# Performance work log

Hardware: AMD Instinct MI355X
Metric: run time of the kernel (lower is better)

Reference implementation:

```python
import jax, jax.numpy as jnp
import numpy as np

EPS = 1e-5

def bn_relu(y, g, b):
    # BatchNorm1d in training mode: stats over (B, L) per channel, biased variance
    mu = jnp.mean(y, axis=(0, 2), keepdims=True)
    var = jnp.var(y, axis=(0, 2), keepdims=True)
    yn = (y - mu) * jax.lax.rsqrt(var + EPS)
    return jax.nn.relu(yn * g[None, :, None] + b[None, :, None])

def conv1x1_pad1(x, W):
    # Conv1d(k=1, padding=1, bias=False): pointwise matmul then zero-pad length by 1 each side
    y = jnp.einsum('bcl,oc->bol', x, W)
    return jnp.pad(y, ((0, 0), (0, 0), (1, 1)))

def conv1x1(x, W, b):
    return jnp.einsum('bcl,oc->bol', x, W) + b[None, :, None]

def conv3_pad1(x, W):
    # Conv1d(k=3, padding=1, bias=False); W: [O, C, 3]
    return jax.lax.conv_general_dilated(x, W, window_strides=(1,), padding=((1, 1),),
                                        dimension_numbers=('NCH', 'OIH', 'NCH'))

def pam(f, Wq, bq, Wk, bk, Wv, bv, gamma):
    q = conv1x1(f, Wq, bq)          # [B, C//8, L]
    k = conv1x1(f, Wk, bk)          # [B, C//8, L]
    v = conv1x1(f, Wv, bv)          # [B, C, L]
    energy = jnp.einsum('bql,bqm->blm', q, k)   # [B, L, L]
    attn = jax.nn.softmax(energy, axis=-1)
    out = jnp.einsum('bcm,blm->bcl', v, attn)
    return gamma * out + f

def cam(f, gamma):
    energy = jnp.einsum('bcl,bdl->bcd', f, f)    # [B, C, C]
    energy_new = jnp.max(energy, axis=-1, keepdims=True) - energy
    attn = jax.nn.softmax(energy_new, axis=-1)
    out = jnp.einsum('bcd,bdl->bcl', attn, f)
    return gamma * out + f

def setup_inputs() -> dict:
    key = jax.random.key(0)
    ks = jax.random.split(key, 24)
    B, C, L = 8, 256, 2046
    IC, OC = C // 4, 128  # inter_channels=64, out_channels
    s = 0.05
    d = {
        'x':   jax.random.normal(ks[0], (B, C, L), jnp.float32),
        'W5a': jax.random.normal(ks[1], (IC, C), jnp.float32) * s,
        'g5a': jnp.ones((IC,), jnp.float32), 'b5a': jnp.zeros((IC,), jnp.float32),
        'W5c': jax.random.normal(ks[2], (IC, C), jnp.float32) * s,
        'g5c': jnp.ones((IC,), jnp.float32), 'b5c': jnp.zeros((IC,), jnp.float32),
        'Wq':  jax.random.normal(ks[3], (IC // 8, IC), jnp.float32) * s,
        'bq':  jnp.zeros((IC // 8,), jnp.float32),
        'Wk':  jax.random.normal(ks[4], (IC // 8, IC), jnp.float32) * s,
        'bk':  jnp.zeros((IC // 8,), jnp.float32),
        'Wv':  jax.random.normal(ks[5], (IC, IC), jnp.float32) * s,
        'bv':  jnp.zeros((IC,), jnp.float32),
        'gamma_pam': jnp.full((1,), 0.1, jnp.float32),
        'gamma_cam': jnp.full((1,), 0.1, jnp.float32),
        'W51': jax.random.normal(ks[6], (IC, IC, 3), jnp.float32) * s,
        'g51': jnp.ones((IC,), jnp.float32), 'b51': jnp.zeros((IC,), jnp.float32),
        'W52': jax.random.normal(ks[7], (IC, IC, 3), jnp.float32) * s,
        'g52': jnp.ones((IC,), jnp.float32), 'b52': jnp.zeros((IC,), jnp.float32),
        'W6':  jax.random.normal(ks[8], (OC, IC), jnp.float32) * s,
        'b6':  jnp.zeros((OC,), jnp.float32),
        'W7':  jax.random.normal(ks[9], (OC, IC), jnp.float32) * s,
        'b7':  jnp.zeros((OC,), jnp.float32),
        'W8':  jax.random.normal(ks[10], (OC, IC), jnp.float32) * s,
        'b8':  jnp.zeros((OC,), jnp.float32),
    }
    return d

def reference(x, W5a, g5a, b5a, W5c, g5c, b5c, Wq, bq, Wk, bk, Wv, bv,
              gamma_pam, gamma_cam, W51, g51, b51, W52, g52, b52,
              W6, b6, W7, b7, W8, b8):
    # dropout (p=0.1) treated as identity (eval mode)
    feat1 = bn_relu(conv1x1_pad1(x, W5a), g5a, b5a)          # [B, IC, L+2]
    sa_feat = pam(feat1, Wq, bq, Wk, bk, Wv, bv, gamma_pam)
    sa_conv = bn_relu(conv3_pad1(sa_feat, W51), g51, b51)
    sa_output = conv1x1(sa_conv, W6, b6)                     # [B, OC, L+2]
    feat2 = bn_relu(conv1x1_pad1(x, W5c), g5c, b5c)
    sc_feat = cam(feat2, gamma_cam)
    sc_conv = bn_relu(conv3_pad1(sc_feat, W52), g52, b52)
    sc_output = conv1x1(sc_conv, W7, b7)
    feat_sum = sa_conv + sc_conv
    sasc = conv1x1(feat_sum, W8, b8)
    # pool == 'maxpool' selects AdaptiveAvgPool1d(1) in the original (note swap)
    sasc = jnp.mean(sasc, axis=-1)                            # [B, OC]
    return (sasc, sa_output, sc_output)
```

## Files before the change

kernel.cpp:

```cpp
#include <hip/hip_runtime.h>
#include <math.h>

#define B 8
#define C 256
#define L 2046
#define LP 2048
#define IC 64
#define OC 128
#define BN_EPS 1e-5f
#define INVN (1.f / 16384.f)

#define OFF_Y1T    0u
#define OFF_Y2C    524288u
#define OFF_Y51T   2097152u
#define OFF_Y52T   2621440u
#define OFF_VB     3145728u
#define OFF_QT     3670016u
#define OFF_KT     3735552u
#define OFF_LPART  3801088u
#define OFF_EPART  3866624u
#define OFF_ATTN   4390912u
#define OFF_STATS1 4423680u
#define OFF_STATS2 4424704u
#define OFF_W5BF   4425728u
#define OFF_W67    4442112u
#define OFF_WT     4450304u
#define OFF_WQKV   4462592u
#define OFF_BQKV   4465152u

typedef __attribute__((ext_vector_type(8))) short bshort8;
typedef __attribute__((ext_vector_type(4))) float f32x4;

__device__ __forceinline__ unsigned short f2bf(float f) {
    union { float f; unsigned int u; } v; v.f = f;
    return (unsigned short)((v.u + 0x8000u) >> 16);
}
__device__ __forceinline__ float bf2f(unsigned short u) {
    union { unsigned int i; float f; } v; v.i = ((unsigned int)u) << 16;
    return v.f;
}
__device__ __forceinline__ unsigned int pk2(float a, float b) {
    union { float f; unsigned int u; } va, vb; va.f = a; vb.f = b;
    return __builtin_amdgcn_perm(vb.u + 0x8000u, va.u + 0x8000u, 0x07060302u);
}

__device__ __forceinline__ void load_coef(const float* __restrict__ STATS,
        const float* __restrict__ g, const float* __restrict__ beta,
        int base, int cnt, float* cA, float* cB) {
    int t = threadIdx.x;
    if (t < cnt) {
        int ch = base + t;
        float s = STATS[ch * 2] + STATS[256 + ch * 2] + STATS[512 + ch * 2] + STATS[768 + ch * 2];
        float q = STATS[ch * 2 + 1] + STATS[256 + ch * 2 + 1] + STATS[512 + ch * 2 + 1] + STATS[768 + ch * 2 + 1];
        float mu = s * INVN;
        float var = q * INVN - mu * mu;
        float A = g[t] * rsqrtf(var + BN_EPS);
        cA[t] = A;
        cB[t] = beta[t] - mu * A;
    }
}

__global__ __launch_bounds__(256) void k_wprep(
        const float* __restrict__ W5a, const float* __restrict__ W5c,
        const float* __restrict__ W6, const float* __restrict__ W7,
        const float* __restrict__ W51, const float* __restrict__ W52,
        const float* __restrict__ Wq, const float* __restrict__ Wk,
        const float* __restrict__ Wv, const float* __restrict__ bq,
        const float* __restrict__ bk, const float* __restrict__ bv,
        const float* __restrict__ b8,
        unsigned short* __restrict__ W5BF, unsigned short* __restrict__ W67,
        unsigned short* __restrict__ WT, unsigned short* __restrict__ WQKV,
        float* __restrict__ BQKV, float* __restrict__ STATS1,
        float* __restrict__ STATS2, float* __restrict__ out_sasc) {
    int i = blockIdx.x * 256 + threadIdx.x;
    if (i < 32768) {
        int o = i >> 8, c = i & 255;
        W5BF[i] = f2bf(o < 64 ? W5a[o * 256 + c] : W5c[(o - 64) * 256 + c]);
    } else if (i < 49152) {
        int j = i - 32768; int g = j >> 13; int r = j & 8191;
        W67[j] = f2bf(g ? W7[r] : W6[r]);
    } else if (i < 73728) {
        int j = i - 49152;
        int c = j & 63, o = (j >> 6) & 63, wt = j >> 12; int w = wt / 3, t = wt % 3;
        const float* Ws = w ? W52 : W51;
        WT[j] = f2bf(Ws[(o * 64 + c) * 3 + t]);
    } else if (i < 78848) {
        int j = i - 73728; int o = j >> 6, c = j & 63;
        float v = o < 8 ? Wq[o * 64 + c] : (o < 16 ? Wk[(o - 8) * 64 + c] : Wv[(o - 16) * 64 + c]);
        WQKV[j] = f2bf(v);
    } else if (i < 78928) {
        int o = i - 78848;
        BQKV[o] = o < 8 ? bq[o] : (o < 16 ? bk[o - 8] : bv[o - 16]);
    } else if (i < 80976) {
        int j = i - 78928;
        if (j < 1024) STATS1[j] = 0.f; else STATS2[j - 1024] = 0.f;
    } else if (i < 82000) {
        int j = i - 80976;
        out_sasc[j] = b8[j & 127];
    }
}

__global__ __launch_bounds__(256) void k_conv1(const float* __restrict__ x,
        const unsigned short* __restrict__ W5BF,
        unsigned short* __restrict__ Y1T, unsigned short* __restrict__ Y2C,
        float* __restrict__ STATS1) {
    __shared__ unsigned short xt[64][264];
    __shared__ float lds_part[4][64];
    int lt = blockIdx.x, b = blockIdx.y;
    int l0 = lt * 64;
    int t = threadIdx.x;
    {
        int j = t & 63, cg = t >> 6;
        int ls = l0 - 1 + j;
        bool ok = (ls >= 0) && (ls < L);
        const float* xs = x + (size_t)(b * C + cg * 64) * L + ls;
        unsigned short* row = &xt[j][cg * 64];
#pragma unroll
        for (int c8 = 0; c8 < 8; ++c8) {
            unsigned int pk[4];
#pragma unroll
            for (int i = 0; i < 4; ++i) {
                float v0 = ok ? xs[(size_t)(c8 * 8 + 2 * i) * L] : 0.f;
                float v1 = ok ? xs[(size_t)(c8 * 8 + 2 * i + 1) * L] : 0.f;
                pk[i] = pk2(v0, v1);
            }
            *(uint4*)(row + c8 * 8) = *(const uint4*)pk;
        }
    }
    __syncthreads();
    int w = t >> 6, lane = t & 63, n = lane & 15, quad = lane >> 4;
    bshort8 wf[2][8];
#pragma unroll
    for (int oi = 0; oi < 2; ++oi)
#pragma unroll
        for (int kt = 0; kt < 8; ++kt)
            wf[oi][kt] = *(const bshort8*)(W5BF + (size_t)((w * 2 + oi) * 16 + n) * C + kt * 32 + quad * 8);
    f32x4 acc[2][4];
#pragma unroll
    for (int oi = 0; oi < 2; ++oi)
#pragma unroll
        for (int sub = 0; sub < 4; ++sub) acc[oi][sub] = (f32x4){0.f, 0.f, 0.f, 0.f};
#pragma unroll
    for (int sub = 0; sub < 4; ++sub) {
        int lloc = sub * 16 + n;
#pragma unroll
        for (int kt = 0; kt < 8; ++kt) {
            bshort8 xb = *(const bshort8*)(&xt[lloc][kt * 32 + quad * 8]);
            acc[0][sub] = __builtin_amdgcn_mfma_f32_16x16x32_bf16(wf[0][kt], xb, acc[0][sub], 0, 0, 0);
            acc[1][sub] = __builtin_amdgcn_mfma_f32_16x16x32_bf16(wf[1][kt], xb, acc[1][sub], 0, 0, 0);
        }
    }
    if (w < 2) {
#pragma unroll
        for (int sub = 0; sub < 4; ++sub) {
            int lp = l0 + sub * 16 + n;
#pragma unroll
            for (int oi = 0; oi < 2; ++oi) {
                int ot = w * 2 + oi;
                uint2 pv;
                pv.x = pk2(acc[oi][sub][0], acc[oi][sub][1]);
                pv.y = pk2(acc[oi][sub][2], acc[oi][sub][3]);
                *(uint2*)(Y1T + ((size_t)(b * LP + lp)) * IC + ot * 16 + quad * 4) = pv;
            }
        }
    } else {
#pragma unroll
        for (int oi = 0; oi < 2; ++oi) {
            int ot = (w - 2) * 2 + oi;
#pragma unroll
            for (int r = 0; r < 4; ++r) {
                int o = ot * 16 + quad * 4 + r;
                unsigned short* dst = Y2C + ((size_t)(b * IC + o)) * LP + l0;
#pragma unroll
                for (int sub = 0; sub < 4; ++sub)
                    dst[sub * 16 + n] = f2bf(acc[oi][sub][r]);
            }
        }
    }
#pragma unroll
    for (int oi = 0; oi < 2; ++oi)
#pragma unroll
        for (int r = 0; r < 4; ++r) {
            float s = 0.f, q = 0.f;
#pragma unroll
            for (int sub = 0; sub < 4; ++sub) {
                float v = acc[oi][sub][r];
                s += v; q += v * v;
            }
#pragma unroll
            for (int msk = 1; msk < 16; msk <<= 1) {
                s += __shfl_xor(s, msk, 64);
                q += __shfl_xor(q, msk, 64);
            }
            if (n == 0) {
                int ci = oi * 16 + quad * 4 + r;
                lds_part[w][ci * 2] = s;
                lds_part[w][ci * 2 + 1] = q;
            }
        }
    __syncthreads();
    {
        int ch = t >> 1, wsrc = ch >> 5;
        int idx = ((ch & 31) << 1) | (t & 1);
        atomicAdd(&STATS1[(blockIdx.x & 3) * 256 + t], lds_part[wsrc][idx]);
    }
}

__device__ void role_qkv(char* dynsm, int lt, int b,
        const unsigned short* __restrict__ Y1T, const float* __restrict__ STATS1,
        const float* __restrict__ g5a, const float* __restrict__ b5a,
        const unsigned short* __restrict__ WQKV, const float* __restrict__ BQKV,
        unsigned short* __restrict__ QT, unsigned short* __restrict__ KT,
        unsigned short* __restrict__ VB) {
    float* cA = (float*)dynsm;
    float* cB = cA + 64;
    load_coef(STATS1, g5a, b5a, 0, 64, cA, cB);
    __syncthreads();
    int t = threadIdx.x;
    int w = t >> 6, lane = t & 63, n = lane & 15, quad = lane >> 4;
    int lrow = lt * 64 + w * 16 + n;
    bshort8 fb[2];
#pragma unroll
    for (int kt = 0; kt < 2; ++kt) {
        bshort8 raw = *(const bshort8*)(Y1T + ((size_t)(b * LP + lrow)) * IC + kt * 32 + quad * 8);
        bshort8 f;
#pragma unroll
        for (int j = 0; j < 8; ++j) {
            int c = kt * 32 + quad * 8 + j;
            float v = fmaxf(fmaf(cA[c], bf2f((unsigned short)raw[j]), cB[c]), 0.f);
            ((unsigned short*)&f)[j] = f2bf(v);
        }
        fb[kt] = f;
    }
    f32x4 acc[5];
#pragma unroll
    for (int ot = 0; ot < 5; ++ot) {
        f32x4 a = {0.f, 0.f, 0.f, 0.f};
#pragma unroll
        for (int kt = 0; kt < 2; ++kt) {
            bshort8 wf = *(const bshort8*)(WQKV + (size_t)(ot * 16 + n) * IC + kt * 32 + quad * 8);
            a = __builtin_amdgcn_mfma_f32_16x16x32_bf16(wf, fb[kt], a, 0, 0, 0);
        }
        acc[ot] = a;
    }
#pragma unroll
    for (int ot = 0; ot < 5; ++ot)
#pragma unroll
        for (int r = 0; r < 4; ++r) {
            int o = ot * 16 + quad * 4 + r;
            unsigned short bv16 = f2bf(acc[ot][r] + BQKV[o]);
            if (ot == 0) {
                if (o < 8) QT[((size_t)(b * LP + lrow)) * 8 + o] = bv16;
                else KT[((size_t)(b * LP + lrow)) * 8 + (o - 8)] = bv16;
            } else {
                VB[((size_t)(b * IC + (o - 16))) * LP + lrow] = bv16;
            }
        }
}

__device__ void role_gram(char* dynsm, int blk, int b,
        const unsigned short* __restrict__ Y2C, const float* __restrict__ STATS1,
        const float* __restrict__ g5c, const float* __restrict__ b5c,
        float* __restrict__ EPART) {
    float* cA = (float*)dynsm;
    float* cB = cA + 64;
    load_coef(STATS1, g5c, b5c, 64, 64, cA, cB);
    __syncthreads();
    int t = threadIdx.x;
    int w = t >> 6, lane = t & 63, n = lane & 15, quad = lane >> 4;
    f32x4 acc[4][4];
#pragma unroll
    for (int ti = 0; ti < 4; ++ti)
#pragma unroll
        for (int tj = 0; tj < 4; ++tj) acc[ti][tj] = (f32x4){0.f, 0.f, 0.f, 0.f};
    for (int chunk = 0; chunk < 4; ++chunk) {
        int lb = (blk * 4 + w) * 128 + chunk * 32 + quad * 8;
        bshort8 frag[4];
#pragma unroll
        for (int g = 0; g < 4; ++g) {
            int c = g * 16 + n;
            bshort8 raw = *(const bshort8*)(Y2C + ((size_t)(b * IC + c)) * LP + lb);
            bshort8 f;
            float A = cA[c], Bc = cB[c];
#pragma unroll
            for (int j = 0; j < 8; ++j)
                ((unsigned short*)&f)[j] = f2bf(fmaxf(fmaf(A, bf2f((unsigned short)raw[j]), Bc), 0.f));
            frag[g] = f;
        }
#pragma unroll
        for (int ti = 0; ti < 4; ++ti)
#pragma unroll
            for (int tj = 0; tj < 4; ++tj)
                acc[ti][tj] = __builtin_amdgcn_mfma_f32_16x16x32_bf16(frag[ti], frag[tj], acc[ti][tj], 0, 0, 0);
    }
    float* ep = EPART + ((size_t)(b * 16 + blk * 4 + w)) * 4096;
#pragma unroll
    for (int ti = 0; ti < 4; ++ti)
#pragma unroll
        for (int tj = 0; tj < 4; ++tj)
#pragma unroll
            for (int r = 0; r < 4; ++r)
                ep[(ti * 16 + quad * 4 + r) * 64 + tj * 16 + n] = acc[ti][tj][r];
}

__global__ __launch_bounds__(256) void k_fuse1(
        const unsigned short* __restrict__ Y1T, const unsigned short* __restrict__ Y2C,
        const float* __restrict__ STATS1,
        const float* __restrict__ g5a, const float* __restrict__ b5a,
        const float* __restrict__ g5c, const float* __restrict__ b5c,
        const unsigned short* __restrict__ WQKV, const float* __restrict__ BQKV,
        unsigned short* __restrict__ QT, unsigned short* __restrict__ KT,
        unsigned short* __restrict__ VB, float* __restrict__ EPART) {
    extern __shared__ char dynsm[];
    int idx = blockIdx.x;
    if (idx < 256) role_qkv(dynsm, idx & 31, idx >> 5, Y1T, STATS1, g5a, b5a,
                            WQKV, BQKV, QT, KT, VB);
    else { int g = idx - 256; role_gram(dynsm, g & 3, g >> 2, Y2C, STATS1, g5c, b5c, EPART); }
}

__device__ void role_pam(char* dynsm, int qt, int ks, int b,
        const unsigned short* __restrict__ qT, const unsigned short* __restrict__ kT,
        const unsigned short* __restrict__ vb,
        unsigned short* __restrict__ OPART, float* __restrict__ LPART) {
    unsigned short* vs0 = (unsigned short*)dynsm;
    unsigned short* vs1 = vs0 + 4608;
    unsigned short* ps  = vs1 + 4608;
    float* os = (float*)dynsm;
    int l0 = qt * 64;
    int tid = threadIdx.x;
    int wq = tid >> 6, lane = tid & 63, n = lane & 15, quad = lane >> 4;
    int srow = tid >> 2, schn = tid & 3;
    bshort8 qa = {};
    if (quad == 0)
        qa = *(const bshort8*)(qT + ((size_t)(b * LP + l0 + wq * 16 + n)) * 8);
    f32x4 acc[4];
#pragma unroll
    for (int s = 0; s < 4; ++s) acc[s] = (f32x4){0.f, 0.f, 0.f, 0.f};
    float li[4] = {0.f, 0.f, 0.f, 0.f};
    unsigned short* pw = ps + wq * 16 * 72;

    {
        const unsigned short* src = vb + ((size_t)(b * IC + srow)) * LP + ks * 512 + schn * 16;
        unsigned short* d = vs0 + srow * 72 + schn * 16;
        *(bshort8*)d = *(const bshort8*)src;
        *(bshort8*)(d + 8) = *(const bshort8*)(src + 8);
    }
    __syncthreads();
    for (int it = 0; it < 8; ++it) {
        unsigned short* cur = (it & 1) ? vs1 : vs0;
        unsigned short* nxt = (it & 1) ? vs0 : vs1;
        if (it < 7) {
            const unsigned short* src = vb + ((size_t)(b * IC + srow)) * LP + ks * 512 + (it + 1) * 64 + schn * 16;
            unsigned short* d = nxt + srow * 72 + schn * 16;
            *(bshort8*)d = *(const bshort8*)src;
            *(bshort8*)(d + 8) = *(const bshort8*)(src + 8);
        }
        int m0 = ks * 512 + it * 64;
        bshort8 kb[4];
#pragma unroll
        for (int s = 0; s < 4; ++s) kb[s] = (bshort8){};
        if (quad == 0) {
#pragma unroll
            for (int s = 0; s < 4; ++s)
                kb[s] = *(const bshort8*)(kT + ((size_t)(b * LP + m0 + s * 16 + n)) * 8);
        }
        f32x4 sc[4];
#pragma unroll
        for (int s = 0; s < 4; ++s)
            sc[s] = __builtin_amdgcn_mfma_f32_16x16x32_bf16(qa, kb[s],
                        (f32x4){0.f, 0.f, 0.f, 0.f}, 0, 0, 0);
#pragma unroll
        for (int s = 0; s < 4; ++s)
#pragma unroll
            for (int r = 0; r < 4; ++r) {
                float p = __expf(sc[s][r]);
                li[r] += p;
                pw[(quad * 4 + r) * 72 + s * 16 + n] = f2bf(p);
            }
#pragma unroll
        for (int step = 0; step < 2; ++step) {
            bshort8 pa = *(const bshort8*)(pw + n * 72 + step * 32 + quad * 8);
#pragma unroll
            for (int s = 0; s < 4; ++s) {
                bshort8 vf = *(const bshort8*)(cur + (s * 16 + n) * 72 + step * 32 + quad * 8);
                acc[s] = __builtin_amdgcn_mfma_f32_16x16x32_bf16(pa, vf, acc[s], 0, 0, 0);
            }
        }
        __syncthreads();
    }
#pragma unroll
    for (int s = 0; s < 4; ++s)
#pragma unroll
        for (int r = 0; r < 4; ++r)
            os[(s * 16 + n) * 65 + wq * 16 + quad * 4 + r] = acc[s][r];
    size_t lbase = ((size_t)((b * 32 + qt) * 4 + ks)) * 64;
#pragma unroll
    for (int r = 0; r < 4; ++r) {
        float s_ = li[r];
#pragma unroll
        for (int msk = 1; msk < 16; msk <<= 1) s_ += __shfl_xor(s_, msk, 64);
        if (n == 0) LPART[lbase + wq * 16 + quad * 4 + r] = s_;
    }
    __syncthreads();
    size_t ob = ((size_t)((b * 32 + qt) * 4 + ks)) * 4096;
    int c = tid >> 2, qc = tid & 3;
    unsigned int* od = (unsigned int*)(OPART + ob + c * 64 + qc * 16);
#pragma unroll
    for (int i = 0; i < 8; ++i)
        od[i] = pk2(os[c * 65 + qc * 16 + 2 * i], os[c * 65 + qc * 16 + 2 * i + 1]);
}

__device__ void role_cam_softmax(char* dynsm, int b,
        const float* __restrict__ EPART, float* __restrict__ attn) {
    float* e = (float*)dynsm;
    int t = threadIdx.x;
    for (int idx = t; idx < 4096; idx += 256) {
        float s = 0.f;
        for (int ch = 0; ch < 16; ++ch) s += EPART[((size_t)(b * 16 + ch)) * 4096 + idx];
        e[idx] = s;
    }
    __syncthreads();
    if (t < 64) {
        float mn = INFINITY;
        for (int d = 0; d < 64; ++d) mn = fminf(mn, e[t * 64 + d]);
        float s = 0.f;
        float* a = attn + (size_t)b * 4096 + t * 64;
        for (int d = 0; d < 64; ++d) { float p = __expf(mn - e[t * 64 + d]); a[d] = p; s += p; }
        float inv = 1.f / s;
        for (int d = 0; d < 64; ++d) a[d] *= inv;
    }
}

__global__ __launch_bounds__(256) void k_fuse2(
        const unsigned short* __restrict__ QT, const unsigned short* __restrict__ KT,
        const unsigned short* __restrict__ VB,
        unsigned short* __restrict__ OPART, float* __restrict__ LPART,
        const float* __restrict__ EPART, float* __restrict__ ATTN) {
    extern __shared__ char dynsm[];
    int idx = blockIdx.x;
    if (idx < 1024) role_pam(dynsm, idx & 31, (idx >> 5) & 3, idx >> 7, QT, KT, VB, OPART, LPART);
    else role_cam_softmax(dynsm, idx - 1024, EPART, ATTN);
}

__device__ __forceinline__ void conv3_from_tile(const unsigned short* tile,
        const unsigned short* __restrict__ WT, unsigned short* __restrict__ dst,
        int b, int l0, float* lds_part, float* __restrict__ STATS2,
        int og, int blockx) {
    int t = threadIdx.x;
    int w = t >> 6, lane = t & 63, n = lane & 15, quad = lane >> 4;
    int lrow = l0 + w * 16 + n;
    f32x4 acc[4];
#pragma unroll
    for (int ot = 0; ot < 4; ++ot) acc[ot] = (f32x4){0.f, 0.f, 0.f, 0.f};
#pragma unroll
    for (int t3 = 0; t3 < 3; ++t3) {
        int trow = w * 16 + n + t3;
        bshort8 fb0 = *(const bshort8*)(tile + trow * 72 + quad * 8);
        bshort8 fb1 = *(const bshort8*)(tile + trow * 72 + 32 + quad * 8);
#pragma unroll
        for (int ot = 0; ot < 4; ++ot) {
            bshort8 w0 = *(const bshort8*)(WT + ((size_t)(t3 * 64 + ot * 16 + n)) * IC + quad * 8);
            bshort8 w1 = *(const bshort8*)(WT + ((size_t)(t3 * 64 + ot * 16 + n)) * IC + 32 + quad * 8);
            acc[ot] = __builtin_amdgcn_mfma_f32_16x16x32_bf16(w0, fb0, acc[ot], 0, 0, 0);
            acc[ot] = __builtin_amdgcn_mfma_f32_16x16x32_bf16(w1, fb1, acc[ot], 0, 0, 0);
        }
    }
#pragma unroll
    for (int ot = 0; ot < 4; ++ot) {
        uint2 pv;
        pv.x = pk2(acc[ot][0], acc[ot][1]);
        pv.y = pk2(acc[ot][2], acc[ot][3]);
        *(uint2*)(dst + ((size_t)(b * LP + lrow)) * IC + ot * 16 + quad * 4) = pv;
    }
#pragma unroll
    for (int ot = 0; ot < 4; ++ot)
#pragma unroll
        for (int r = 0; r < 4; ++r) {
            float s = acc[ot][r], q = s * s;
#pragma unroll
            for (int msk = 1; msk < 16; msk <<= 1) {
                s += __shfl_xor(s, msk, 64);
                q += __shfl_xor(q, msk, 64);
            }
            if (n == 0) {
                int cch = ot * 16 + quad * 4 + r;
                lds_part[w * 128 + cch * 2] = s;
                lds_part[w * 128 + cch * 2 + 1] = q;
            }
        }
    __syncthreads();
    if (t < 128) {
        float s = lds_part[t] + lds_part[128 + t] + lds_part[256 + t] + lds_part[384 + t];
        atomicAdd(&STATS2[(blockx & 3) * 256 + og * 128 + t], s);
    }
}

__device__ void role_pam_c3(char* dynsm, int qt, int b,
        const unsigned short* __restrict__ OPART, const float* __restrict__ LPART,
        const unsigned short* __restrict__ Y1T, const float* __restrict__ STATS1,
        const float* __restrict__ g5a, const float* __restrict__ b5a,
        const float* __restrict__ gamma, const unsigned short* __restrict__ WT,
        unsigned short* __restrict__ Y51T, float* __restrict__ STATS2) {
    float* dn = (float*)dynsm;
    float* cA = dn + 64; float* cB = cA + 64;
    unsigned short* tile = (unsigned short*)(cB + 64);
    float* lds_part = (float*)(tile + 4752);
    int l0 = qt * 64;
    int t = threadIdx.x;
    load_coef(STATS1, g5a, b5a, 0, 64, cA, cB);
    if (t < 64) {
        size_t lbase = ((size_t)((b * 32 + qt) * 4)) * 64;
        dn[t] = LPART[lbase + t] + LPART[lbase + 64 + t] +
                LPART[lbase + 128 + t] + LPART[lbase + 192 + t];
    }
    __syncthreads();
    float gm = gamma[0];
    {
        int c = t >> 2, qc = t & 3;
        float O[16];
#pragma unroll
        for (int i = 0; i < 16; ++i) O[i] = 0.f;
        size_t ob = ((size_t)((b * 32 + qt) * 4)) * 4096 + c * 64 + qc * 16;
#pragma unroll
        for (int s = 0; s < 4; ++s) {
            bshort8 p0 = *(const bshort8*)(OPART + ob + (size_t)s * 4096);
            bshort8 p1 = *(const bshort8*)(OPART + ob + (size_t)s * 4096 + 8);
#pragma unroll
            for (int i = 0; i < 8; ++i) {
                O[i]     += bf2f((unsigned short)p0[i]);
                O[8 + i] += bf2f((unsigned short)p1[i]);
            }
        }
#pragma unroll
        for (int i = 0; i < 16; ++i) {
            int q = qc * 16 + i;
            unsigned short raw = Y1T[((size_t)(b * LP + l0 + q)) * IC + c];
            float f1v = fmaxf(fmaf(cA[c], bf2f(raw), cB[c]), 0.f);
            tile[(1 + q) * 72 + c] = f2bf(fmaf(gm, O[i] / dn[q], f1v));
        }
    }
    if (t < 128) {
        int row = (t & 1) ? 65 : 0;
        int ch = t >> 1;
        int l = l0 - 1 + row;
        float val = 0.f;
        if (l >= 0 && l < LP) {
            int qh = l >> 6, lih = l & 63;
            size_t lb2 = ((size_t)((b * 32 + qh) * 4)) * 64;
            float dnh = LPART[lb2 + lih] + LPART[lb2 + 64 + lih] +
                        LPART[lb2 + 128 + lih] + LPART[lb2 + 192 + lih];
            size_t ob2 = ((size_t)((b * 32 + qh) * 4)) * 4096 + ch * 64 + lih;
            float Oh = bf2f(OPART[ob2]) + bf2f(OPART[ob2 + 4096]) +
                       bf2f(OPART[ob2 + 8192]) + bf2f(OPART[ob2 + 12288]);
            float f1v = fmaxf(fmaf(cA[ch], bf2f(Y1T[((size_t)(b * LP + l)) * IC + ch]), cB[ch]), 0.f);
            val = fmaf(gm, Oh / dnh, f1v);
        }
        tile[row * 72 + ch] = f2bf(val);
    }
    __syncthreads();
    conv3_from_tile(tile, WT, Y51T, b, l0, lds_part, STATS2, 0, qt);
}

__device__ void role_cam_c3(char* dynsm, int lt, int b,
        const float* __restrict__ attn, const unsigned short* __restrict__ Y2C,
        const float* __restrict__ STATS1,
        const float* __restrict__ g5c, const float* __restrict__ b5c,
        const float* __restrict__ gamma, const unsigned short* __restrict__ WT,
        unsigned short* __restrict__ Y52T, float* __restrict__ STATS2) {
    float* as = (float*)dynsm;
    float* cA = as + 4096; float* cB = cA + 64;
    unsigned short* tile = (unsigned short*)(cB + 64);
    float* lds_part = (float*)(tile + 4752);
    int l0 = lt * 64;
    int t = threadIdx.x;
    load_coef(STATS1, g5c, b5c, 64, 64, cA, cB);
    for (int i = t; i < 4096; i += 256) as[i] = attn[(size_t)b * 4096 + i];
    __syncthreads();
    float gm = gamma[0];
    {
        int lq = t & 63, cg = t >> 6;
        const unsigned short* fb = Y2C + (size_t)b * IC * LP + l0 + lq;
        float acc[16];
#pragma unroll
        for (int i = 0; i < 16; ++i) acc[i] = 0.f;
        for (int d4 = 0; d4 < 16; ++d4) {
            float fv[4];
#pragma unroll
            for (int i = 0; i < 4; ++i) {
                int d = 4 * d4 + i;
                fv[i] = fmaxf(fmaf(cA[d], bf2f(fb[(size_t)d * LP]), cB[d]), 0.f);
            }
#pragma unroll
            for (int cc = 0; cc < 16; ++cc) {
                const float4 a4 = *reinterpret_cast<const float4*>(as + (cg * 16 + cc) * 64 + d4 * 4);
                acc[cc] += a4.x * fv[0] + a4.y * fv[1] + a4.z * fv[2] + a4.w * fv[3];
            }
        }
#pragma unroll
        for (int cc = 0; cc < 16; ++cc) {
            int c = cg * 16 + cc;
            float res = fmaxf(fmaf(cA[c], bf2f(fb[(size_t)c * LP]), cB[c]), 0.f);
            tile[(1 + lq) * 72 + c] = f2bf(fmaf(gm, acc[cc], res));
        }
    }
    float* fcol = lds_part;
    if (t < 128) {
        int row = t >> 6;
        int ch = t & 63;
        int l = l0 - 1 + row * 65;
        float v = 0.f;
        if (l >= 0 && l < LP)
            v = fmaxf(fmaf(cA[ch], bf2f(Y2C[(size_t)b * IC * LP + (size_t)ch * LP + l]), cB[ch]), 0.f);
        fcol[row * 64 + ch] = v;
    }
    __syncthreads();
    if (t < 128) {
        int sel = t & 1;
        int row = sel ? 65 : 0;
        int ch = t >> 1;
        int l = l0 - 1 + (sel ? 65 : 0);
        float val = 0.f;
        if (l >= 0 && l < LP) {
            const float* fc = fcol + sel * 64;
            float a = 0.f;
#pragma unroll 8
            for (int d = 0; d < 64; ++d) a = fmaf(as[ch * 64 + d], fc[d], a);
            val = fmaf(gm, a, fc[ch]);
        }
        tile[row * 72 + ch] = f2bf(val);
    }
    __syncthreads();
    conv3_from_tile(tile, WT, Y52T, b, l0, lds_part, STATS2, 1, lt);
}

__global__ __launch_bounds__(256) void k_fuse3c(
        const unsigned short* __restrict__ OPART, const float* __restrict__ LPART,
        const unsigned short* __restrict__ Y1T, const unsigned short* __restrict__ Y2C,
        const float* __restrict__ STATS1,
        const float* __restrict__ g5a, const float* __restrict__ b5a,
        const float* __restrict__ g5c, const float* __restrict__ b5c,
        const float* __restrict__ gpam, const float* __restrict__ gcam,
        const float* __restrict__ ATTN, const unsigned short* __restrict__ WTall,
        unsigned short* __restrict__ Y51T, unsigned short* __restrict__ Y52T,
        float* __restrict__ STATS2) {
    extern __shared__ char dynsm[];
    int idx = blockIdx.x;
    if (idx < 256) role_pam_c3(dynsm, idx & 31, idx >> 5, OPART, LPART, Y1T,
                               STATS1, g5a, b5a, gpam, WTall, Y51T, STATS2);
    else { int g = idx - 256; role_cam_c3(dynsm, g & 31, g >> 5, ATTN, Y2C,
                                          STATS1, g5c, b5c, gcam, WTall + 12288,
                                          Y52T, STATS2); }
}

__global__ __launch_bounds__(256) void k_final(const unsigned short* __restrict__ Y51T,
        const unsigned short* __restrict__ Y52T, const float* __restrict__ STATS2,
        const float* __restrict__ g51, const float* __restrict__ b51,
        const float* __restrict__ g52, const float* __restrict__ b52,
        const unsigned short* __restrict__ W67,
        const float* __restrict__ b6, const float* __restrict__ b7,
        const float* __restrict__ W8,
        float* __restrict__ out_sa, float* __restrict__ out_sc,
        float* __restrict__ out_sasc) {
    __shared__ float cA[128], cB[128];
    __shared__ float fsw[4][64];
    __shared__ float chsum[64];
    int lt = blockIdx.x, og = blockIdx.y, b = blockIdx.z;
    int t = threadIdx.x;
    if (t < 128) {
        float s = STATS2[t * 2] + STATS2[256 + t * 2] + STATS2[512 + t * 2] + STATS2[768 + t * 2];
        float q = STATS2[t * 2 + 1] + STATS2[256 + t * 2 + 1] + STATS2[512 + t * 2 + 1] + STATS2[768 + t * 2 + 1];
        float mu = s * INVN, var = q * INVN - mu * mu;
        float gv = t < 64 ? g51[t] : g52[t - 64];
        float bv = t < 64 ? b51[t] : b52[t - 64];
        float A = gv * rsqrtf(var + BN_EPS);
        cA[t] = A; cB[t] = bv - mu * A;
    }
    __syncthreads();
    int w = t >> 6, lane = t & 63, n = lane & 15, quad = lane >> 4;
    int lrow = lt * 64 + w * 16 + n;
    float fs_lane[16];
    bshort8 ba[2], bb[2];
#pragma unroll
    for (int kt = 0; kt < 2; ++kt) {
        bshort8 ra = *(const bshort8*)(Y51T + ((size_t)(b * LP + lrow)) * IC + kt * 32 + quad * 8);
        bshort8 rb = *(const bshort8*)(Y52T + ((size_t)(b * LP + lrow)) * IC + kt * 32 + quad * 8);
        bshort8 fa, fb;
#pragma unroll
        for (int j = 0; j < 8; ++j) {
            int c = kt * 32 + quad * 8 + j;
            float v1 = fmaxf(fmaf(cA[c], bf2f((unsigned short)ra[j]), cB[c]), 0.f);
            float v2 = fmaxf(fmaf(cA[64 + c], bf2f((unsigned short)rb[j]), cB[64 + c]), 0.f);
            ((unsigned short*)&fa)[j] = f2bf(v1);
            ((unsigned short*)&fb)[j] = f2bf(v2);
            fs_lane[kt * 8 + j] = v1 + v2;
        }
        ba[kt] = fa; bb[kt] = fb;
    }
    f32x4 accA[4], accB[4];
#pragma unroll
    for (int ot = 0; ot < 4; ++ot) {
        accA[ot] = (f32x4){0.f, 0.f, 0.f, 0.f};
        accB[ot] = (f32x4){0.f, 0.f, 0.f, 0.f};
    }
#pragma unroll
    for (int ot = 0; ot < 4; ++ot)
#pragma unroll
        for (int kt = 0; kt < 2; ++kt) {
            bshort8 wa = *(const bshort8*)(W67 + (size_t)(og * 64 + ot * 16 + n) * IC + kt * 32 + quad * 8);
            bshort8 wb = *(const bshort8*)(W67 + 8192 + (size_t)(og * 64 + ot * 16 + n) * IC + kt * 32 + quad * 8);
            accA[ot] = __builtin_amdgcn_mfma_f32_16x16x32_bf16(wa, ba[kt], accA[ot], 0, 0, 0);
            accB[ot] = __builtin_amdgcn_mfma_f32_16x16x32_bf16(wb, bb[kt], accB[ot], 0, 0, 0);
        }
#pragma unroll
    for (int ot = 0; ot < 4; ++ot)
#pragma unroll
        for (int r = 0; r < 4; ++r) {
            int o = og * 64 + ot * 16 + quad * 4 + r;
            out_sa[((size_t)(b * OC + o)) * LP + lrow] = accA[ot][r] + b6[o];
            out_sc[((size_t)(b * OC + o)) * LP + lrow] = accB[ot][r] + b7[o];
        }
    if (og == 0) {
#pragma unroll
        for (int i = 0; i < 16; ++i) {
            float s = fs_lane[i];
#pragma unroll
            for (int msk = 1; msk < 16; msk <<= 1) s += __shfl_xor(s, msk, 64);
            if (n == 0) {
                int c = (i >> 3) * 32 + quad * 8 + (i & 7);
                fsw[w][c] = s;
            }
        }
        __syncthreads();
        if (t < 64) chsum[t] = fsw[0][t] + fsw[1][t] + fsw[2][t] + fsw[3][t];
        __syncthreads();
        if (t < 128) {
            float s = 0.f;
            for (int c = 0; c < 64; ++c) s = fmaf(W8[t * 64 + c], chsum[c], s);
            atomicAdd(&out_sasc[b * OC + t], s * (1.f / (float)LP));
        }
    }
}

extern "C" void kernel_launch(void* const* d_in, const int* in_sizes, int n_in,
                              void* d_out, int out_size, void* d_ws, size_t ws_size,
                              hipStream_t stream) {
    (void)in_sizes; (void)n_in; (void)out_size; (void)ws_size;
    const float* x    = (const float*)d_in[0];
    const float* W5a  = (const float*)d_in[1];
    const float* g5a  = (const float*)d_in[2];
    const float* b5a  = (const float*)d_in[3];
    const float* W5c  = (const float*)d_in[4];
    const float* g5c  = (const float*)d_in[5];
    const float* b5c  = (const float*)d_in[6];
    const float* Wq   = (const float*)d_in[7];
    const float* bq   = (const float*)d_in[8];
    const float* Wk   = (const float*)d_in[9];
    const float* bk   = (const float*)d_in[10];
    const float* Wv   = (const float*)d_in[11];
    const float* bv   = (const float*)d_in[12];
    const float* gpam = (const float*)d_in[13];
    const float* gcam = (const float*)d_in[14];
    const float* W51  = (const float*)d_in[15];
    const float* g51  = (const float*)d_in[16];
    const float* b51  = (const float*)d_in[17];
    const float* W52  = (const float*)d_in[18];
    const float* g52  = (const float*)d_in[19];
    const float* b52  = (const float*)d_in[20];
    const float* W6   = (const float*)d_in[21];
    const float* b6   = (const float*)d_in[22];
    const float* W7   = (const float*)d_in[23];
    const float* b7   = (const float*)d_in[24];
    const float* W8   = (const float*)d_in[25];
    const float* b8   = (const float*)d_in[26];

    float* ws = (float*)d_ws;
    float* out = (float*)d_out;
    unsigned short* Y1T  = (unsigned short*)(ws + OFF_Y1T);
    unsigned short* Y2C  = (unsigned short*)(ws + OFF_Y2C);
    unsigned short* Y51T = (unsigned short*)(ws + OFF_Y51T);
    unsigned short* Y52T = (unsigned short*)(ws + OFF_Y52T);
    unsigned short* VB   = (unsigned short*)(ws + OFF_VB);
    unsigned short* QT   = (unsigned short*)(ws + OFF_QT);
    unsigned short* KT   = (unsigned short*)(ws + OFF_KT);
    float* LPART  = ws + OFF_LPART;
    float* EPART  = ws + OFF_EPART;
    float* ATTN   = ws + OFF_ATTN;
    float* STATS1 = ws + OFF_STATS1;
    float* STATS2 = ws + OFF_STATS2;
    unsigned short* W5BF = (unsigned short*)(ws + OFF_W5BF);
    unsigned short* W67  = (unsigned short*)(ws + OFF_W67);
    unsigned short* WT   = (unsigned short*)(ws + OFF_WT);
    unsigned short* WQKV = (unsigned short*)(ws + OFF_WQKV);
    float* BQKV = ws + OFF_BQKV;

    float* out_sa = out + B * OC;
    float* out_sc = out + B * OC + (size_t)B * OC * LP;
    unsigned short* OPART = (unsigned short*)out_sa;

    k_wprep<<<321, 256, 0, stream>>>(W5a, W5c, W6, W7, W51, W52, Wq, Wk, Wv,
                                     bq, bk, bv, b8, W5BF, W67, WT, WQKV, BQKV,
                                     STATS1, STATS2, out);
    k_conv1<<<dim3(32, B), 256, 0, stream>>>(x, W5BF, Y1T, Y2C, STATS1);
    k_fuse1<<<288, 256, 512, stream>>>(Y1T, Y2C, STATS1, g5a, b5a, g5c, b5c,
                                       WQKV, BQKV, QT, KT, VB, EPART);
    k_fuse2<<<1032, 256, 27648, stream>>>(QT, KT, VB, OPART, LPART, EPART, ATTN);
    k_fuse3c<<<512, 256, 28448, stream>>>(OPART, LPART, Y1T, Y2C, STATS1,
                                          g5a, b5a, g5c, b5c, gpam, gcam, ATTN,
                                          WT, Y51T, Y52T, STATS2);
    k_final<<<dim3(32, 2, B), 256, 0, stream>>>(Y51T, Y52T, STATS2, g51, b51, g52, b52,
                                                W67, b6, b7, W8, out_sa, out_sc, out);
}
```

Measured before the change: 217.5 us.

## Fuse PAM attention with conv3 and CAM softmax into one kernel

Merges the split-K PAM attention kernel and the subsequent conv3 kernel into one role that walks all 2048 keys per 64-row query tile. Tiles overlap by two halo rows (62 useful outputs per tile), which removes the OPART/LPART partial buffers and their reduction. The CAM softmax is also moved into each CAM conv3 block, parallelised across four threads per row, which removes the ATTN buffer and one kernel launch. The trade-off is far fewer attention blocks (272 instead of 1024) with four times the serial work each, plus about 3% of the attention recomputed for the halos, so parallelism drops in exchange for less memory traffic and launch overhead.

```diff
diff --git a/kernel.cpp b/kernel.cpp
--- a/kernel.cpp
+++ b/kernel.cpp
@@ -17,9 +17,7 @@
 #define OFF_VB     3145728u
 #define OFF_QT     3670016u
 #define OFF_KT     3735552u
-#define OFF_LPART  3801088u
 #define OFF_EPART  3866624u
-#define OFF_ATTN   4390912u
 #define OFF_STATS1 4423680u
 #define OFF_STATS2 4424704u
 #define OFF_W5BF   4425728u
@@ -318,130 +316,6 @@
     else { int g = idx - 256; role_gram(dynsm, g & 3, g >> 2, Y2C, STATS1, g5c, b5c, EPART); }
 }
 
-__device__ void role_pam(char* dynsm, int qt, int ks, int b,
-        const unsigned short* __restrict__ qT, const unsigned short* __restrict__ kT,
-        const unsigned short* __restrict__ vb,
-        unsigned short* __restrict__ OPART, float* __restrict__ LPART) {
-    unsigned short* vs0 = (unsigned short*)dynsm;
-    unsigned short* vs1 = vs0 + 4608;
-    unsigned short* ps  = vs1 + 4608;
-    float* os = (float*)dynsm;
-    int l0 = qt * 64;
-    int tid = threadIdx.x;
-    int wq = tid >> 6, lane = tid & 63, n = lane & 15, quad = lane >> 4;
-    int srow = tid >> 2, schn = tid & 3;
-    bshort8 qa = {};
-    if (quad == 0)
-        qa = *(const bshort8*)(qT + ((size_t)(b * LP + l0 + wq * 16 + n)) * 8);
-    f32x4 acc[4];
-#pragma unroll
-    for (int s = 0; s < 4; ++s) acc[s] = (f32x4){0.f, 0.f, 0.f, 0.f};
-    float li[4] = {0.f, 0.f, 0.f, 0.f};
-    unsigned short* pw = ps + wq * 16 * 72;
-
-    {
-        const unsigned short* src = vb + ((size_t)(b * IC + srow)) * LP + ks * 512 + schn * 16;
-        unsigned short* d = vs0 + srow * 72 + schn * 16;
-        *(bshort8*)d = *(const bshort8*)src;
-        *(bshort8*)(d + 8) = *(const bshort8*)(src + 8);
-    }
-    __syncthreads();
-    for (int it = 0; it < 8; ++it) {
-        unsigned short* cur = (it & 1) ? vs1 : vs0;
-        unsigned short* nxt = (it & 1) ? vs0 : vs1;
-        if (it < 7) {
-            const unsigned short* src = vb + ((size_t)(b * IC + srow)) * LP + ks * 512 + (it + 1) * 64 + schn * 16;
-            unsigned short* d = nxt + srow * 72 + schn * 16;
-            *(bshort8*)d = *(const bshort8*)src;
-            *(bshort8*)(d + 8) = *(const bshort8*)(src + 8);
-        }
-        int m0 = ks * 512 + it * 64;
-        bshort8 kb[4];
-#pragma unroll
-        for (int s = 0; s < 4; ++s) kb[s] = (bshort8){};
-        if (quad == 0) {
-#pragma unroll
-            for (int s = 0; s < 4; ++s)
-                kb[s] = *(const bshort8*)(kT + ((size_t)(b * LP + m0 + s * 16 + n)) * 8);
-        }
-        f32x4 sc[4];
-#pragma unroll
-        for (int s = 0; s < 4; ++s)
-            sc[s] = __builtin_amdgcn_mfma_f32_16x16x32_bf16(qa, kb[s],
-                        (f32x4){0.f, 0.f, 0.f, 0.f}, 0, 0, 0);
-#pragma unroll
-        for (int s = 0; s < 4; ++s)
-#pragma unroll
-            for (int r = 0; r < 4; ++r) {
-                float p = __expf(sc[s][r]);
-                li[r] += p;
-                pw[(quad * 4 + r) * 72 + s * 16 + n] = f2bf(p);
-            }
-#pragma unroll
-        for (int step = 0; step < 2; ++step) {
-            bshort8 pa = *(const bshort8*)(pw + n * 72 + step * 32 + quad * 8);
-#pragma unroll
-            for (int s = 0; s < 4; ++s) {
-                bshort8 vf = *(const bshort8*)(cur + (s * 16 + n) * 72 + step * 32 + quad * 8);
-                acc[s] = __builtin_amdgcn_mfma_f32_16x16x32_bf16(pa, vf, acc[s], 0, 0, 0);
-            }
-        }
-        __syncthreads();
-    }
-#pragma unroll
-    for (int s = 0; s < 4; ++s)
-#pragma unroll
-        for (int r = 0; r < 4; ++r)
-            os[(s * 16 + n) * 65 + wq * 16 + quad * 4 + r] = acc[s][r];
-    size_t lbase = ((size_t)((b * 32 + qt) * 4 + ks)) * 64;
-#pragma unroll
-    for (int r = 0; r < 4; ++r) {
-        float s_ = li[r];
-#pragma unroll
-        for (int msk = 1; msk < 16; msk <<= 1) s_ += __shfl_xor(s_, msk, 64);
-        if (n == 0) LPART[lbase + wq * 16 + quad * 4 + r] = s_;
-    }
-    __syncthreads();
-    size_t ob = ((size_t)((b * 32 + qt) * 4 + ks)) * 4096;
-    int c = tid >> 2, qc = tid & 3;
-    unsigned int* od = (unsigned int*)(OPART + ob + c * 64 + qc * 16);
-#pragma unroll
-    for (int i = 0; i < 8; ++i)
-        od[i] = pk2(os[c * 65 + qc * 16 + 2 * i], os[c * 65 + qc * 16 + 2 * i + 1]);
-}
-
-__device__ void role_cam_softmax(char* dynsm, int b,
-        const float* __restrict__ EPART, float* __restrict__ attn) {
-    float* e = (float*)dynsm;
-    int t = threadIdx.x;
-    for (int idx = t; idx < 4096; idx += 256) {
-        float s = 0.f;
-        for (int ch = 0; ch < 16; ++ch) s += EPART[((size_t)(b * 16 + ch)) * 4096 + idx];
-        e[idx] = s;
-    }
-    __syncthreads();
-    if (t < 64) {
-        float mn = INFINITY;
-        for (int d = 0; d < 64; ++d) mn = fminf(mn, e[t * 64 + d]);
-        float s = 0.f;
-        float* a = attn + (size_t)b * 4096 + t * 64;
-        for (int d = 0; d < 64; ++d) { float p = __expf(mn - e[t * 64 + d]); a[d] = p; s += p; }
-        float inv = 1.f / s;
-        for (int d = 0; d < 64; ++d) a[d] *= inv;
-    }
-}
-
-__global__ __launch_bounds__(256) void k_fuse2(
-        const unsigned short* __restrict__ QT, const unsigned short* __restrict__ KT,
-        const unsigned short* __restrict__ VB,
-        unsigned short* __restrict__ OPART, float* __restrict__ LPART,
-        const float* __restrict__ EPART, float* __restrict__ ATTN) {
-    extern __shared__ char dynsm[];
-    int idx = blockIdx.x;
-    if (idx < 1024) role_pam(dynsm, idx & 31, (idx >> 5) & 3, idx >> 7, QT, KT, VB, OPART, LPART);
-    else role_cam_softmax(dynsm, idx - 1024, EPART, ATTN);
-}
-
 __device__ __forceinline__ void conv3_from_tile(const unsigned short* tile,
         const unsigned short* __restrict__ WT, unsigned short* __restrict__ dst,
         int b, int l0, float* lds_part, float* __restrict__ STATS2,
@@ -495,74 +369,182 @@
     }
 }
 
-__device__ void role_pam_c3(char* dynsm, int qt, int b,
-        const unsigned short* __restrict__ OPART, const float* __restrict__ LPART,
+__device__ void role_pam_full(char* dynsm, int qt, int b,
+        const unsigned short* __restrict__ qT, const unsigned short* __restrict__ kT,
+        const unsigned short* __restrict__ vb,
         const unsigned short* __restrict__ Y1T, const float* __restrict__ STATS1,
         const float* __restrict__ g5a, const float* __restrict__ b5a,
         const float* __restrict__ gamma, const unsigned short* __restrict__ WT,
         unsigned short* __restrict__ Y51T, float* __restrict__ STATS2) {
-    float* dn = (float*)dynsm;
-    float* cA = dn + 64; float* cB = cA + 64;
-    unsigned short* tile = (unsigned short*)(cB + 64);
-    float* lds_part = (float*)(tile + 4752);
-    int l0 = qt * 64;
-    int t = threadIdx.x;
+    unsigned short* vs0 = (unsigned short*)dynsm;
+    unsigned short* vs1 = vs0 + 4608;
+    unsigned short* ps  = vs1 + 4608;
+    float* os = (float*)dynsm;
+    unsigned short* tile = ps;
+    float* cA = (float*)(dynsm + 27648);
+    float* cB = cA + 64;
+    float* dn = cB + 64;
+    float* lds_part = dn + 64;
+    int base = qt * 62 - 1;
+    int tid = threadIdx.x;
+    int wq = tid >> 6, lane = tid & 63, n = lane & 15, quad = lane >> 4;
+    int srow = tid >> 2, schn = tid & 3;
     load_coef(STATS1, g5a, b5a, 0, 64, cA, cB);
-    if (t < 64) {
-        size_t lbase = ((size_t)((b * 32 + qt) * 4)) * 64;
-        dn[t] = LPART[lbase + t] + LPART[lbase + 64 + t] +
-                LPART[lbase + 128 + t] + LPART[lbase + 192 + t];
+    int qrow = base + wq * 16 + n;
+    int qcl = qrow < 0 ? 0 : (qrow > LP - 1 ? LP - 1 : qrow);
+    bshort8 qa = {};
+    if (quad == 0)
+        qa = *(const bshort8*)(qT + ((size_t)(b * LP + qcl)) * 8);
+    f32x4 acc[4];
+#pragma unroll
+    for (int s = 0; s < 4; ++s) acc[s] = (f32x4){0.f, 0.f, 0.f, 0.f};
+    float li[4] = {0.f, 0.f, 0.f, 0.f};
+    unsigned short* pw = ps + wq * 16 * 72;
+
+    {
+        const unsigned short* src = vb + ((size_t)(b * IC + srow)) * LP + schn * 16;
+        unsigned short* d = vs0 + srow * 72 + schn * 16;
+        *(bshort8*)d = *(const bshort8*)src;
+        *(bshort8*)(d + 8) = *(const bshort8*)(src + 8);
+    }
+    bshort8 kb[4];
+#pragma unroll
+    for (int s = 0; s < 4; ++s) kb[s] = (bshort8){};
+    if (quad == 0) {
+#pragma unroll
+        for (int s = 0; s < 4; ++s)
+            kb[s] = *(const bshort8*)(kT + ((size_t)(b * LP + s * 16 + n)) * 8);
+    }
+    __syncthreads();
+    for (int it = 0; it < 32; ++it) {
+        unsigned short* cur = (it & 1) ? vs1 : vs0;
+        unsigned short* nxt = (it & 1) ? vs0 : vs1;
+        if (it < 31) {
+            const unsigned short* src = vb + ((size_t)(b * IC + srow)) * LP + (it + 1) * 64 + schn * 16;
+            unsigned short* d = nxt + srow * 72 + schn * 16;
+            *(bshort8*)d = *(const bshort8*)src;
+            *(bshort8*)(d + 8) = *(const bshort8*)(src + 8);
+        }
+        bshort8 kn[4];
+#pragma unroll
+        for (int s = 0; s < 4; ++s) kn[s] = (bshort8){};
+        if (it < 31 && quad == 0) {
+            int m1 = (it + 1) * 64;
+#pragma unroll
+            for (int s = 0; s < 4; ++s)
+                kn[s] = *(const bshort8*)(kT + ((size_t)(b * LP + m1 + s * 16 + n)) * 8);
+        }
+        f32x4 sc[4];
+#pragma unroll
+        for (int s = 0; s < 4; ++s)
+            sc[s] = __builtin_amdgcn_mfma_f32_16x16x32_bf16(qa, kb[s],
+                        (f32x4){0.f, 0.f, 0.f, 0.f}, 0, 0, 0);
+#pragma unroll
+        for (int s = 0; s < 4; ++s)
+#pragma unroll
+            for (int r = 0; r < 4; ++r) {
+                float p = __expf(sc[s][r]);
+                li[r] += p;
+                pw[(quad * 4 + r) * 72 + s * 16 + n] = f2bf(p);
+            }
+#pragma unroll
+        for (int step = 0; step < 2; ++step) {
+            bshort8 pa = *(const bshort8*)(pw + n * 72 + step * 32 + quad * 8);
+#pragma unroll
+            for (int s = 0; s < 4; ++s) {
+                bshort8 vf = *(const bshort8*)(cur + (s * 16 + n) * 72 + step * 32 + quad * 8);
+                acc[s] = __builtin_amdgcn_mfma_f32_16x16x32_bf16(pa, vf, acc[s], 0, 0, 0);
+            }
+        }
+        __syncthreads();
+#pragma unroll
+        for (int s = 0; s < 4; ++s) kb[s] = kn[s];
+    }
+#pragma unroll
+    for (int s = 0; s < 4; ++s)
+#pragma unroll
+        for (int r = 0; r < 4; ++r)
+            os[(s * 16 + n) * 65 + wq * 16 + quad * 4 + r] = acc[s][r];
+#pragma unroll
+    for (int r = 0; r < 4; ++r) {
+        float s_ = li[r];
+#pragma unroll
+        for (int msk = 1; msk < 16; msk <<= 1) s_ += __shfl_xor(s_, msk, 64);
+        if (n == 0) dn[wq * 16 + quad * 4 + r] = s_;
     }
     __syncthreads();
     float gm = gamma[0];
     {
-        int c = t >> 2, qc = t & 3;
-        float O[16];
-#pragma unroll
-        for (int i = 0; i < 16; ++i) O[i] = 0.f;
-        size_t ob = ((size_t)((b * 32 + qt) * 4)) * 4096 + c * 64 + qc * 16;
-#pragma unroll
-        for (int s = 0; s < 4; ++s) {
-            bshort8 p0 = *(const bshort8*)(OPART + ob + (size_t)s * 4096);
-            bshort8 p1 = *(const bshort8*)(OPART + ob + (size_t)s * 4096 + 8);
-#pragma unroll
-            for (int i = 0; i < 8; ++i) {
-                O[i]     += bf2f((unsigned short)p0[i]);
-                O[8 + i] += bf2f((unsigned short)p1[i]);
-            }
-        }
+        int c = tid >> 2, qc = tid & 3;
 #pragma unroll
         for (int i = 0; i < 16; ++i) {
-            int q = qc * 16 + i;
-            unsigned short raw = Y1T[((size_t)(b * LP + l0 + q)) * IC + c];
-            float f1v = fmaxf(fmaf(cA[c], bf2f(raw), cB[c]), 0.f);
-            tile[(1 + q) * 72 + c] = f2bf(fmaf(gm, O[i] / dn[q], f1v));
-        }
-    }
-    if (t < 128) {
-        int row = (t & 1) ? 65 : 0;
-        int ch = t >> 1;
-        int l = l0 - 1 + row;
-        float val = 0.f;
-        if (l >= 0 && l < LP) {
-            int qh = l >> 6, lih = l & 63;
-            size_t lb2 = ((size_t)((b * 32 + qh) * 4)) * 64;
-            float dnh = LPART[lb2 + lih] + LPART[lb2 + 64 + lih] +
-                        LPART[lb2 + 128 + lih] + LPART[lb2 + 192 + lih];
-            size_t ob2 = ((size_t)((b * 32 + qh) * 4)) * 4096 + ch * 64 + lih;
-            float Oh = bf2f(OPART[ob2]) + bf2f(OPART[ob2 + 4096]) +
-                       bf2f(OPART[ob2 + 8192]) + bf2f(OPART[ob2 + 12288]);
-            float f1v = fmaxf(fmaf(cA[ch], bf2f(Y1T[((size_t)(b * LP + l)) * IC + ch]), cB[ch]), 0.f);
-            val = fmaf(gm, Oh / dnh, f1v);
-        }
-        tile[row * 72 + ch] = f2bf(val);
-    }
-    __syncthreads();
-    conv3_from_tile(tile, WT, Y51T, b, l0, lds_part, STATS2, 0, qt);
-}
-
-__device__ void role_cam_c3(char* dynsm, int lt, int b,
-        const float* __restrict__ attn, const unsigned short* __restrict__ Y2C,
+            int r = qc * 16 + i;
+            int absr = base + r;
+            float val = 0.f;
+            if (absr >= 0 && absr < LP) {
+                unsigned short raw = Y1T[((size_t)(b * LP + absr)) * IC + c];
+                float f1v = fmaxf(fmaf(cA[c], bf2f(raw), cB[c]), 0.f);
+                val = fmaf(gm, os[c * 65 + r] / dn[r], f1v);
+            }
+            tile[r * 72 + c] = f2bf(val);
+        }
+    }
+    __syncthreads();
+    {
+        int j = wq * 16 + n;
+        int absout = base + 1 + j;
+        bool valid = (j < 62) && (absout < LP);
+        f32x4 a3[4];
+#pragma unroll
+        for (int ot = 0; ot < 4; ++ot) a3[ot] = (f32x4){0.f, 0.f, 0.f, 0.f};
+#pragma unroll
+        for (int t3 = 0; t3 < 3; ++t3) {
+            bshort8 fb0 = *(const bshort8*)(tile + (j + t3) * 72 + quad * 8);
+            bshort8 fb1 = *(const bshort8*)(tile + (j + t3) * 72 + 32 + quad * 8);
+#pragma unroll
+            for (int ot = 0; ot < 4; ++ot) {
+                bshort8 w0 = *(const bshort8*)(WT + ((size_t)(t3 * 64 + ot * 16 + n)) * IC + quad * 8);
+                bshort8 w1 = *(const bshort8*)(WT + ((size_t)(t3 * 64 + ot * 16 + n)) * IC + 32 + quad * 8);
+                a3[ot] = __builtin_amdgcn_mfma_f32_16x16x32_bf16(w0, fb0, a3[ot], 0, 0, 0);
+                a3[ot] = __builtin_amdgcn_mfma_f32_16x16x32_bf16(w1, fb1, a3[ot], 0, 0, 0);
+            }
+        }
+        if (valid) {
+#pragma unroll
+            for (int ot = 0; ot < 4; ++ot) {
+                uint2 pv;
+                pv.x = pk2(a3[ot][0], a3[ot][1]);
+                pv.y = pk2(a3[ot][2], a3[ot][3]);
+                *(uint2*)(Y51T + ((size_t)(b * LP + absout)) * IC + ot * 16 + quad * 4) = pv;
+            }
+        }
+#pragma unroll
+        for (int ot = 0; ot < 4; ++ot)
+#pragma unroll
+            for (int r = 0; r < 4; ++r) {
+                float s = valid ? a3[ot][r] : 0.f;
+                float q = s * s;
+#pragma unroll
+                for (int msk = 1; msk < 16; msk <<= 1) {
+                    s += __shfl_xor(s, msk, 64);
+                    q += __shfl_xor(q, msk, 64);
+                }
+                if (n == 0) {
+                    int cch = ot * 16 + quad * 4 + r;
+                    lds_part[wq * 128 + cch * 2] = s;
+                    lds_part[wq * 128 + cch * 2 + 1] = q;
+                }
+            }
+        __syncthreads();
+        if (tid < 128) {
+            float s = lds_part[tid] + lds_part[128 + tid] + lds_part[256 + tid] + lds_part[384 + tid];
+            atomicAdd(&STATS2[(qt & 3) * 256 + tid], s);
+        }
+    }
+}
+
+__device__ void role_cam_full(char* dynsm, int lt, int b,
+        const float* __restrict__ EPART, const unsigned short* __restrict__ Y2C,
         const float* __restrict__ STATS1,
         const float* __restrict__ g5c, const float* __restrict__ b5c,
         const float* __restrict__ gamma, const unsigned short* __restrict__ WT,
@@ -574,7 +556,32 @@
     int l0 = lt * 64;
     int t = threadIdx.x;
     load_coef(STATS1, g5c, b5c, 64, 64, cA, cB);
-    for (int i = t; i < 4096; i += 256) as[i] = attn[(size_t)b * 4096 + i];
+    for (int idx = t; idx < 4096; idx += 256) {
+        float s = 0.f;
+#pragma unroll
+        for (int ch = 0; ch < 16; ++ch) s += EPART[((size_t)(b * 16 + ch)) * 4096 + idx];
+        as[idx] = s;
+    }
+    __syncthreads();
+    {
+        int row = t >> 2, qd = t & 3;
+        float v[16];
+#pragma unroll
+        for (int i = 0; i < 16; ++i) v[i] = as[row * 64 + qd * 16 + i];
+        float mn = v[0];
+#pragma unroll
+        for (int i = 1; i < 16; ++i) mn = fminf(mn, v[i]);
+        mn = fminf(mn, __shfl_xor(mn, 1, 64));
+        mn = fminf(mn, __shfl_xor(mn, 2, 64));
+        float s = 0.f;
+#pragma unroll
+        for (int i = 0; i < 16; ++i) { v[i] = __expf(mn - v[i]); s += v[i]; }
+        s += __shfl_xor(s, 1, 64);
+        s += __shfl_xor(s, 2, 64);
+        float inv = 1.f / s;
+#pragma unroll
+        for (int i = 0; i < 16; ++i) as[row * 64 + qd * 16 + i] = v[i] * inv;
+    }
     __syncthreads();
     float gm = gamma[0];
     {
@@ -633,23 +640,28 @@
     conv3_from_tile(tile, WT, Y52T, b, l0, lds_part, STATS2, 1, lt);
 }
 
-__global__ __launch_bounds__(256) void k_fuse3c(
-        const unsigned short* __restrict__ OPART, const float* __restrict__ LPART,
+__global__ __launch_bounds__(256) void k_fuse2(
+        const unsigned short* __restrict__ QT, const unsigned short* __restrict__ KT,
+        const unsigned short* __restrict__ VB,
         const unsigned short* __restrict__ Y1T, const unsigned short* __restrict__ Y2C,
         const float* __restrict__ STATS1,
         const float* __restrict__ g5a, const float* __restrict__ b5a,
         const float* __restrict__ g5c, const float* __restrict__ b5c,
         const float* __restrict__ gpam, const float* __restrict__ gcam,
-        const float* __restrict__ ATTN, const unsigned short* __restrict__ WTall,
+        const float* __restrict__ EPART, const unsigned short* __restrict__ WTall,
         unsigned short* __restrict__ Y51T, unsigned short* __restrict__ Y52T,
         float* __restrict__ STATS2) {
     extern __shared__ char dynsm[];
     int idx = blockIdx.x;
-    if (idx < 256) role_pam_c3(dynsm, idx & 31, idx >> 5, OPART, LPART, Y1T,
-                               STATS1, g5a, b5a, gpam, WTall, Y51T, STATS2);
-    else { int g = idx - 256; role_cam_c3(dynsm, g & 31, g >> 5, ATTN, Y2C,
-                                          STATS1, g5c, b5c, gcam, WTall + 12288,
-                                          Y52T, STATS2); }
+    if (idx < 272) {
+        int b = idx / 34; int qt = idx - b * 34;
+        role_pam_full(dynsm, qt, b, QT, KT, VB, Y1T, STATS1, g5a, b5a, gpam,
+                      WTall, Y51T, STATS2);
+    } else {
+        int g = idx - 272;
+        role_cam_full(dynsm, g & 31, g >> 5, EPART, Y2C, STATS1, g5c, b5c, gcam,
+                      WTall + 12288, Y52T, STATS2);
+    }
 }
 
 __global__ __launch_bounds__(256) void k_final(const unsigned short* __restrict__ Y51T,
@@ -782,9 +794,7 @@
     unsigned short* VB   = (unsigned short*)(ws + OFF_VB);
     unsigned short* QT   = (unsigned short*)(ws + OFF_QT);
     unsigned short* KT   = (unsigned short*)(ws + OFF_KT);
-    float* LPART  = ws + OFF_LPART;
     float* EPART  = ws + OFF_EPART;
-    float* ATTN   = ws + OFF_ATTN;
     float* STATS1 = ws + OFF_STATS1;
     float* STATS2 = ws + OFF_STATS2;
     unsigned short* W5BF = (unsigned short*)(ws + OFF_W5BF);
@@ -795,7 +805,6 @@
 
     float* out_sa = out + B * OC;
     float* out_sc = out + B * OC + (size_t)B * OC * LP;
-    unsigned short* OPART = (unsigned short*)out_sa;
 
     k_wprep<<<321, 256, 0, stream>>>(W5a, W5c, W6, W7, W51, W52, Wq, Wk, Wv,
                                      bq, bk, bv, b8, W5BF, W67, WT, WQKV, BQKV,
@@ -803,10 +812,9 @@
     k_conv1<<<dim3(32, B), 256, 0, stream>>>(x, W5BF, Y1T, Y2C, STATS1);
     k_fuse1<<<288, 256, 512, stream>>>(Y1T, Y2C, STATS1, g5a, b5a, g5c, b5c,
                                        WQKV, BQKV, QT, KT, VB, EPART);
-    k_fuse2<<<1032, 256, 27648, stream>>>(QT, KT, VB, OPART, LPART, EPART, ATTN);
-    k_fuse3c<<<512, 256, 28448, stream>>>(OPART, LPART, Y1T, Y2C, STATS1,
-                                          g5a, b5a, g5c, b5c, gpam, gcam, ATTN,
-                                          WT, Y51T, Y52T, STATS2);
+    k_fuse2<<<528, 256, 30464, stream>>>(QT, KT, VB, Y1T, Y2C, STATS1,
+                                         g5a, b5a, g5c, b5c, gpam, gcam,
+                                         EPART, WT, Y51T, Y52T, STATS2);
     k_final<<<dim3(32, 2, B), 256, 0, stream>>>(Y51T, Y52T, STATS2, g51, b51, g52, b52,
                                                 W67, b6, b7, W8, out_sa, out_sc, out);
 }
```

Measured after the change: 220.5 us. Within noise of the previous version (+1.4%).
